# Kernel optimization log

Hardware: AMD Instinct MI355X
Metric: run time of the kernel (lower is better)

The kernel has to match this reference:

```python
import jax, jax.numpy as jnp
import numpy as np
from jax import lax

T, H, F, E, K = 4096, 1024, 2048, 8, 2

def setup_inputs() -> dict:
    key = jax.random.key(0)
    k1, k2, k3, k4 = jax.random.split(key, 4)
    return {
        "hidden_states": jax.random.normal(k1, (T, H), jnp.float32),
        "gate_w": jax.random.normal(k2, (E, H), jnp.float32) * 0.02,
        "w1": jax.random.normal(k3, (E, 2 * F, H), jnp.float32) * 0.02,  # fused gate+up
        "w2": jax.random.normal(k4, (E, H, F), jnp.float32) * 0.02,      # down proj
        "top_k": K,
    }

def reference(hidden_states, gate_w, w1, w2, top_k):
    tokens = hidden_states.shape[0]
    # Router gate (Linear, no bias)
    router_logits = hidden_states @ gate_w.T                     # [T, E]
    probs = jax.nn.softmax(router_logits.astype(jnp.float32), axis=-1)
    topk_w, topk_idx = lax.top_k(probs, top_k)                   # [T, K]
    topk_w = topk_w / jnp.sum(topk_w, axis=-1, keepdims=True)    # renormalize
    # Dense combine weights [T, E] (zero for unselected experts)
    combine = jnp.zeros_like(probs).at[jnp.arange(tokens)[:, None], topk_idx].add(topk_w)
    combine = combine.astype(hidden_states.dtype)

    def expert_step(acc, ew):
        w1_e, w2_e, c_e = ew                                     # [2F,H], [H,F], [T]
        h = hidden_states @ w1_e.T                               # [T, 2F]
        g, u = jnp.split(h, 2, axis=-1)
        y = (jax.nn.silu(g) * u) @ w2_e.T                        # [T, H]
        return acc + c_e[:, None] * y, None

    acc0 = jnp.zeros_like(hidden_states)
    final_hidden_states, _ = lax.scan(expert_step, acc0, (w1, w2, combine.T))
    return final_hidden_states, router_logits
```

## Files before the change

kernel.cpp:

```cpp
#include <hip/hip_runtime.h>

#define T 4096
#define Hdim 1024
#define Fdim 2048
#define NE 8
#define TOPK 2
#define TK (T*TOPK)

typedef unsigned short ushort_t;
typedef __attribute__((ext_vector_type(8))) short bf16x8;
typedef __attribute__((ext_vector_type(4))) float floatx4;

__device__ __forceinline__ ushort_t f2bf(float f) {
    unsigned u = __float_as_uint(f);
    u += 0x7fff + ((u >> 16) & 1);
    return (ushort_t)(u >> 16);
}
__device__ __forceinline__ uint4 cvt8(const float4 a, const float4 b) {
    uint4 r;
    r.x = (unsigned)f2bf(a.x) | ((unsigned)f2bf(a.y) << 16);
    r.y = (unsigned)f2bf(a.z) | ((unsigned)f2bf(a.w) << 16);
    r.z = (unsigned)f2bf(b.x) | ((unsigned)f2bf(b.y) << 16);
    r.w = (unsigned)f2bf(b.z) | ((unsigned)f2bf(b.w) << 16);
    return r;
}
__device__ __forceinline__ void gld16(const ushort_t* g, short* l) {
    __builtin_amdgcn_global_load_lds((const __attribute__((address_space(1))) void*)g,
                                     (__attribute__((address_space(3))) void*)l, 16, 0, 0);
}

__global__ __launch_bounds__(256) void cvt2_kernel(
    const float* __restrict__ srcA, ushort_t* __restrict__ dstA, long n8A,
    const float* __restrict__ srcB, ushort_t* __restrict__ dstB)
{
    long i = (long)blockIdx.x * 256 + threadIdx.x;
    if (i < n8A) {
        float4 a = *(const float4*)(srcA + i * 8);
        float4 b = *(const float4*)(srcA + i * 8 + 4);
        *(uint4*)(dstA + i * 8) = cvt8(a, b);
    } else {
        long j = i - n8A;
        float4 a = *(const float4*)(srcB + j * 8);
        float4 b = *(const float4*)(srcB + j * 8 + 4);
        *(uint4*)(dstB + j * 8) = cvt8(a, b);
    }
}

__global__ __launch_bounds__(256) void cvt_kernel(const float* __restrict__ src,
                                                  ushort_t* __restrict__ dst)
{
    long i = (long)blockIdx.x * 256 + threadIdx.x;
    float4 a = *(const float4*)(src + i * 8);
    float4 b = *(const float4*)(src + i * 8 + 4);
    *(uint4*)(dst + i * 8) = cvt8(a, b);
}

__global__ __launch_bounds__(64) void router_kernel(
    const float* __restrict__ hs, const float* __restrict__ gw,
    float* __restrict__ logits_out,
    int2* __restrict__ choice, float2* __restrict__ cwt, int* __restrict__ counts)
{
    const int t = blockIdx.x;
    const int lane = threadIdx.x;
    if (t == 0 && lane < NE) counts[lane] = 0;

    float hreg[16];
#pragma unroll
    for (int i = 0; i < 16; ++i)
        hreg[i] = hs[(long)t * Hdim + lane + 64 * i];

    float acc[NE];
#pragma unroll
    for (int e = 0; e < NE; ++e) {
        float s = 0.f;
#pragma unroll
        for (int i = 0; i < 16; ++i)
            s += hreg[i] * gw[e * Hdim + lane + 64 * i];
#pragma unroll
        for (int off = 32; off > 0; off >>= 1)
            s += __shfl_xor(s, off, 64);
        acc[e] = s;
    }

    if (lane < NE) logits_out[t * NE + lane] = acc[lane];

    if (lane == 0) {
        int i1 = 0;
#pragma unroll
        for (int e = 1; e < NE; ++e) if (acc[e] > acc[i1]) i1 = e;
        int i2 = -1;
#pragma unroll
        for (int e = 0; e < NE; ++e) {
            if (e == i1) continue;
            if (i2 < 0 || acc[e] > acc[i2]) i2 = e;
        }
        float p2 = __expf(acc[i2] - acc[i1]);
        float z  = 1.f + p2;
        choice[t] = make_int2(i1, i2);
        cwt[t]    = make_float2(1.f / z, p2 / z);
    }
}

__global__ __launch_bounds__(256) void scatter_kernel(
    const int2* __restrict__ choice, const float2* __restrict__ cwt,
    int* __restrict__ counts, int* __restrict__ tok_slot, float* __restrict__ tok_wt)
{
    __shared__ int lhist[NE];
    __shared__ int lbase[NE];
    __shared__ int lpos[NE];
    const int tid = threadIdx.x;
    if (tid < NE) { lhist[tid] = 0; lpos[tid] = 0; }
    __syncthreads();

    const int t = blockIdx.x * 256 + tid;
    int2   ch = choice[t];
    float2 wv = cwt[t];
    atomicAdd(&lhist[ch.x], 1);
    atomicAdd(&lhist[ch.y], 1);
    __syncthreads();

    if (tid < NE) lbase[tid] = atomicAdd(&counts[tid], lhist[tid]);
    __syncthreads();

    int p1 = atomicAdd(&lpos[ch.x], 1);
    int p2 = atomicAdd(&lpos[ch.y], 1);
    int o1 = lbase[ch.x] + p1;
    int o2 = lbase[ch.y] + p2;
    tok_slot[ch.x * T + o1] = t * TOPK + 0;
    tok_wt [ch.x * T + o1] = wv.x;
    tok_slot[ch.y * T + o2] = t * TOPK + 1;
    tok_wt [ch.y * T + o2] = wv.y;
}

__global__ __launch_bounds__(256) void gemm1_kernel(
    const ushort_t* __restrict__ hsb, const ushort_t* __restrict__ w1b,
    const int* __restrict__ counts, const int* __restrict__ tok_slot,
    ushort_t* __restrict__ actb)
{
    const int e = blockIdx.z;
    const int cnt = counts[e];
    const int row0 = blockIdx.y * 128;
    if (row0 >= cnt) return;
    const int f0 = blockIdx.x * 64;

    __shared__ short As[128 * 32];
    __shared__ short Bs[128 * 32];
    __shared__ int slotLds[128];

    const int tid = threadIdx.x;
    if (tid < 128) {
        int idx = row0 + tid;
        slotLds[tid] = (idx < cnt) ? tok_slot[e * T + idx] : -1;
    }
    __syncthreads();

    const int rA0 = tid >> 2,      rA1 = 64 + (tid >> 2);
    const int seg = (tid & 3) * 8;
    int s0 = slotLds[rA0], s1 = slotLds[rA1];
    const ushort_t* srcA0 = hsb + (long)((s0 >= 0 ? (s0 >> 1) : 0)) * Hdim + seg;
    const ushort_t* srcA1 = hsb + (long)((s1 >= 0 ? (s1 >> 1) : 0)) * Hdim + seg;
    const ushort_t* srcB0 = w1b + ((long)e * 2 * Fdim + (f0 + rA0)) * Hdim + seg;
    const ushort_t* srcB1 = w1b + ((long)e * 2 * Fdim + Fdim + (f0 + rA0)) * Hdim + seg;

    const int lane = tid & 63;
    const int w = tid >> 6;
    const int wm = (w >> 1) * 64;
    const int wn = (w & 1) * 32;
    const int fr = lane & 15, fg = lane >> 4;

    floatx4 accg[4][2] = {};
    floatx4 accu[4][2] = {};

    for (int k0 = 0; k0 < Hdim; k0 += 32) {
        __syncthreads();
        gld16(srcA0 + k0, &As[tid * 8]);
        gld16(srcA1 + k0, &As[(256 + tid) * 8]);
        gld16(srcB0 + k0, &Bs[tid * 8]);
        gld16(srcB1 + k0, &Bs[(256 + tid) * 8]);
        __syncthreads();

        bf16x8 a[4], g[2], u[2];
#pragma unroll
        for (int ms = 0; ms < 4; ++ms)
            a[ms] = *(bf16x8*)&As[(wm + ms * 16 + fr) * 32 + fg * 8];
#pragma unroll
        for (int ns = 0; ns < 2; ++ns) {
            g[ns] = *(bf16x8*)&Bs[(wn + ns * 16 + fr) * 32 + fg * 8];
            u[ns] = *(bf16x8*)&Bs[(64 + wn + ns * 16 + fr) * 32 + fg * 8];
        }
#pragma unroll
        for (int ms = 0; ms < 4; ++ms)
#pragma unroll
            for (int ns = 0; ns < 2; ++ns) {
                accg[ms][ns] = __builtin_amdgcn_mfma_f32_16x16x32_bf16(a[ms], g[ns], accg[ms][ns], 0, 0, 0);
                accu[ms][ns] = __builtin_amdgcn_mfma_f32_16x16x32_bf16(a[ms], u[ns], accu[ms][ns], 0, 0, 0);
            }
    }

#pragma unroll
    for (int ms = 0; ms < 4; ++ms)
#pragma unroll
        for (int ns = 0; ns < 2; ++ns)
#pragma unroll
            for (int j = 0; j < 4; ++j) {
                int m = wm + ms * 16 + fg * 4 + j;
                int slot = slotLds[m];
                if (slot >= 0) {
                    int fcol = f0 + wn + ns * 16 + fr;
                    float gv = accg[ms][ns][j];
                    float uv = accu[ms][ns][j];
                    float av = (gv / (1.f + __expf(-gv))) * uv;
                    actb[(long)slot * Fdim + fcol] = f2bf(av);
                }
            }
}

__global__ __launch_bounds__(512) void gemm2_kernel(
    const ushort_t* __restrict__ actb, const ushort_t* __restrict__ w2b,
    const int* __restrict__ counts, const int* __restrict__ tok_slot,
    const float* __restrict__ tok_wt, float* __restrict__ partial)
{
    const int e = blockIdx.z;
    const int cnt = counts[e];
    const int row0 = blockIdx.y * 128;
    if (row0 >= cnt) return;
    const int h0 = blockIdx.x * 128;

    __shared__ short As[128 * 32];
    __shared__ short Bs[128 * 32];
    __shared__ int   slotLds[128];
    __shared__ float wtLds[128];

    const int tid = threadIdx.x;
    if (tid < 128) {
        int idx = row0 + tid;
        bool ok = idx < cnt;
        slotLds[tid] = ok ? tok_slot[e * T + idx] : -1;
        wtLds[tid]   = ok ? tok_wt [e * T + idx] : 0.f;
    }
    __syncthreads();

    const int r   = tid >> 2;
    const int seg = (tid & 3) * 8;
    int s = slotLds[r];
    const ushort_t* srcA = actb + (long)(s >= 0 ? s : 0) * Fdim + seg;
    const ushort_t* srcB = w2b + ((long)e * Hdim + (h0 + r)) * Fdim + seg;

    const int lane = tid & 63;
    const int w = tid >> 6;
    const int wm = (w >> 2) * 64;
    const int wn = (w & 3) * 32;
    const int fr = lane & 15, fg = lane >> 4;

    floatx4 acc[4][2] = {};

    for (int k0 = 0; k0 < Fdim; k0 += 32) {
        __syncthreads();
        gld16(srcA + k0, &As[tid * 8]);
        gld16(srcB + k0, &Bs[tid * 8]);
        __syncthreads();

        bf16x8 a[4], b[2];
#pragma unroll
        for (int ms = 0; ms < 4; ++ms)
            a[ms] = *(bf16x8*)&As[(wm + ms * 16 + fr) * 32 + fg * 8];
#pragma unroll
        for (int ns = 0; ns < 2; ++ns)
            b[ns] = *(bf16x8*)&Bs[(wn + ns * 16 + fr) * 32 + fg * 8];
#pragma unroll
        for (int ms = 0; ms < 4; ++ms)
#pragma unroll
            for (int ns = 0; ns < 2; ++ns)
                acc[ms][ns] = __builtin_amdgcn_mfma_f32_16x16x32_bf16(a[ms], b[ns], acc[ms][ns], 0, 0, 0);
    }

#pragma unroll
    for (int ms = 0; ms < 4; ++ms)
#pragma unroll
        for (int ns = 0; ns < 2; ++ns)
#pragma unroll
            for (int j = 0; j < 4; ++j) {
                int m = wm + ms * 16 + fg * 4 + j;
                int slot = slotLds[m];
                if (slot >= 0) {
                    int hcol = h0 + wn + ns * 16 + fr;
                    partial[(long)slot * Hdim + hcol] = acc[ms][ns][j] * wtLds[m];
                }
            }
}

__global__ __launch_bounds__(256) void combine_kernel(
    const float* __restrict__ partial, float* __restrict__ out)
{
    long i = (long)blockIdx.x * 256 + threadIdx.x;
    int t  = (int)(i / (Hdim / 4));
    int h4 = (int)(i % (Hdim / 4));
    const float4 p0 = *(const float4*)&partial[(long)(2 * t    ) * Hdim + h4 * 4];
    const float4 p1 = *(const float4*)&partial[(long)(2 * t + 1) * Hdim + h4 * 4];
    float4 s;
    s.x = p0.x + p1.x; s.y = p0.y + p1.y; s.z = p0.z + p1.z; s.w = p0.w + p1.w;
    *(float4*)&out[(long)t * Hdim + h4 * 4] = s;
}

extern "C" void kernel_launch(void* const* d_in, const int* in_sizes, int n_in,
                              void* d_out, int out_size, void* d_ws, size_t ws_size,
                              hipStream_t stream)
{
    const float* hs = (const float*)d_in[0];
    const float* gw = (const float*)d_in[1];
    const float* w1 = (const float*)d_in[2];
    const float* w2 = (const float*)d_in[3];

    float* out        = (float*)d_out;
    float* logits_out = out + (long)T * Hdim;

    char* ws = (char*)d_ws;
    size_t off = 0;
    int* counts = (int*)(ws + off);          off += 256;
    int* tok_slot = (int*)(ws + off);        off += (size_t)NE * T * sizeof(int);
    float* tok_wt = (float*)(ws + off);      off += (size_t)NE * T * sizeof(float);
    off = (off + 255) & ~(size_t)255;
    ushort_t* hsb = (ushort_t*)(ws + off);   off += (size_t)T * Hdim * sizeof(ushort_t);
    off = (off + 255) & ~(size_t)255;
    char* w1region = ws + off;               off += (size_t)NE * 2 * Fdim * Hdim * sizeof(ushort_t);
    ushort_t* w1b = (ushort_t*)w1region;
    ushort_t* w2b = (ushort_t*)w1region;
    float* partial = (float*)(w1region + (size_t)NE * Hdim * Fdim * sizeof(ushort_t));
    off = (off + 255) & ~(size_t)255;
    ushort_t* actb = (ushort_t*)(ws + off);  off += (size_t)TK * Fdim * sizeof(ushort_t);
    int2*   choice = (int2*)actb;
    float2* cwt    = (float2*)((char*)actb + (size_t)T * sizeof(int2));

    const long n8_hs = (long)T * Hdim / 8;
    const long n8_w1 = (long)NE * 2 * Fdim * Hdim / 8;
    const long n8_w2 = (long)NE * Hdim * Fdim / 8;

    cvt2_kernel<<<(int)((n8_hs + n8_w1) / 256), 256, 0, stream>>>(hs, hsb, n8_hs, w1, w1b);
    router_kernel<<<T, 64, 0, stream>>>(hs, gw, logits_out, choice, cwt, counts);
    scatter_kernel<<<T / 256, 256, 0, stream>>>(choice, cwt, counts, tok_slot, tok_wt);
    gemm1_kernel<<<dim3(Fdim / 64, T / 128, NE), 256, 0, stream>>>(hsb, w1b, counts, tok_slot, actb);
    cvt_kernel<<<(int)(n8_w2 / 256), 256, 0, stream>>>(w2, w2b);
    gemm2_kernel<<<dim3(Hdim / 128, T / 128, NE), 512, 0, stream>>>(actb, w2b, counts, tok_slot, tok_wt, partial);
    combine_kernel<<<(int)((long)T * Hdim / 4 / 256), 256, 0, stream>>>(partial, out);
}
```

Before: 437.3 us.

## Split-K the down-projection GEMM with atomic accumulation and retile its warps

The down-projection GEMM now splits the F reduction into two halves, each handled by its own block, and accumulates results into the partial buffer with float atomics. The partial buffer is zeroed in the same kernel that converts w2 to bf16. Blocks drop from 512 to 256 threads, with each warp computing a 64x64 sub-tile instead of 64x32, so each thread loads two rows of the A and B tiles. The gate/up GEMM is also issued as two launches over halves of F. The aim is more parallel blocks and more MFMA reuse per LDS load, at the cost of atomic traffic, an extra 32MB zeroing pass and more accumulator registers.

```diff
diff --git a/kernel.cpp b/kernel.cpp
--- a/kernel.cpp
+++ b/kernel.cpp
@@ -46,13 +46,21 @@
     }
 }
 
-__global__ __launch_bounds__(256) void cvt_kernel(const float* __restrict__ src,
-                                                  ushort_t* __restrict__ dst)
+__global__ __launch_bounds__(256) void cvtw2_zero_kernel(
+    const float* __restrict__ src, ushort_t* __restrict__ dst, long n8,
+    float* __restrict__ partial)
 {
     long i = (long)blockIdx.x * 256 + threadIdx.x;
-    float4 a = *(const float4*)(src + i * 8);
-    float4 b = *(const float4*)(src + i * 8 + 4);
-    *(uint4*)(dst + i * 8) = cvt8(a, b);
+    if (i < n8) {
+        float4 a = *(const float4*)(src + i * 8);
+        float4 b = *(const float4*)(src + i * 8 + 4);
+        *(uint4*)(dst + i * 8) = cvt8(a, b);
+    } else {
+        long j = i - n8;
+        float4 z = make_float4(0.f, 0.f, 0.f, 0.f);
+        *(float4*)(partial + j * 8)     = z;
+        *(float4*)(partial + j * 8 + 4) = z;
+    }
 }
 
 __global__ __launch_bounds__(64) void router_kernel(
@@ -135,13 +143,13 @@
 __global__ __launch_bounds__(256) void gemm1_kernel(
     const ushort_t* __restrict__ hsb, const ushort_t* __restrict__ w1b,
     const int* __restrict__ counts, const int* __restrict__ tok_slot,
-    ushort_t* __restrict__ actb)
+    ushort_t* __restrict__ actb, int f_base)
 {
     const int e = blockIdx.z;
     const int cnt = counts[e];
     const int row0 = blockIdx.y * 128;
     if (row0 >= cnt) return;
-    const int f0 = blockIdx.x * 64;
+    const int f0 = f_base + blockIdx.x * 64;
 
     __shared__ short As[128 * 32];
     __shared__ short Bs[128 * 32];
@@ -215,7 +223,7 @@
             }
 }
 
-__global__ __launch_bounds__(512) void gemm2_kernel(
+__global__ __launch_bounds__(256) void gemm2_kernel(
     const ushort_t* __restrict__ actb, const ushort_t* __restrict__ w2b,
     const int* __restrict__ counts, const int* __restrict__ tok_slot,
     const float* __restrict__ tok_wt, float* __restrict__ partial)
@@ -224,7 +232,9 @@
     const int cnt = counts[e];
     const int row0 = blockIdx.y * 128;
     if (row0 >= cnt) return;
-    const int h0 = blockIdx.x * 128;
+    const int ks = blockIdx.x & 1;
+    const int h0 = (blockIdx.x >> 1) * 128;
+    const int kbase = ks * (Fdim / 2);
 
     __shared__ short As[128 * 32];
     __shared__ short Bs[128 * 32];
@@ -240,51 +250,55 @@
     }
     __syncthreads();
 
-    const int r   = tid >> 2;
+    const int rA0 = tid >> 2, rA1 = 64 + (tid >> 2);
     const int seg = (tid & 3) * 8;
-    int s = slotLds[r];
-    const ushort_t* srcA = actb + (long)(s >= 0 ? s : 0) * Fdim + seg;
-    const ushort_t* srcB = w2b + ((long)e * Hdim + (h0 + r)) * Fdim + seg;
+    int s0 = slotLds[rA0], s1 = slotLds[rA1];
+    const ushort_t* srcA0 = actb + (long)(s0 >= 0 ? s0 : 0) * Fdim + kbase + seg;
+    const ushort_t* srcA1 = actb + (long)(s1 >= 0 ? s1 : 0) * Fdim + kbase + seg;
+    const ushort_t* srcB0 = w2b + ((long)e * Hdim + (h0 + rA0)) * Fdim + kbase + seg;
+    const ushort_t* srcB1 = w2b + ((long)e * Hdim + (h0 + rA1)) * Fdim + kbase + seg;
 
     const int lane = tid & 63;
     const int w = tid >> 6;
-    const int wm = (w >> 2) * 64;
-    const int wn = (w & 3) * 32;
+    const int wm = (w >> 1) * 64;
+    const int wn = (w & 1) * 64;
     const int fr = lane & 15, fg = lane >> 4;
 
-    floatx4 acc[4][2] = {};
-
-    for (int k0 = 0; k0 < Fdim; k0 += 32) {
+    floatx4 acc[4][4] = {};
+
+    for (int k0 = 0; k0 < Fdim / 2; k0 += 32) {
         __syncthreads();
-        gld16(srcA + k0, &As[tid * 8]);
-        gld16(srcB + k0, &Bs[tid * 8]);
+        gld16(srcA0 + k0, &As[tid * 8]);
+        gld16(srcA1 + k0, &As[(256 + tid) * 8]);
+        gld16(srcB0 + k0, &Bs[tid * 8]);
+        gld16(srcB1 + k0, &Bs[(256 + tid) * 8]);
         __syncthreads();
 
-        bf16x8 a[4], b[2];
+        bf16x8 a[4], b[4];
 #pragma unroll
         for (int ms = 0; ms < 4; ++ms)
             a[ms] = *(bf16x8*)&As[(wm + ms * 16 + fr) * 32 + fg * 8];
 #pragma unroll
-        for (int ns = 0; ns < 2; ++ns)
+        for (int ns = 0; ns < 4; ++ns)
             b[ns] = *(bf16x8*)&Bs[(wn + ns * 16 + fr) * 32 + fg * 8];
 #pragma unroll
         for (int ms = 0; ms < 4; ++ms)
 #pragma unroll
-            for (int ns = 0; ns < 2; ++ns)
+            for (int ns = 0; ns < 4; ++ns)
                 acc[ms][ns] = __builtin_amdgcn_mfma_f32_16x16x32_bf16(a[ms], b[ns], acc[ms][ns], 0, 0, 0);
     }
 
 #pragma unroll
     for (int ms = 0; ms < 4; ++ms)
 #pragma unroll
-        for (int ns = 0; ns < 2; ++ns)
+        for (int ns = 0; ns < 4; ++ns)
 #pragma unroll
             for (int j = 0; j < 4; ++j) {
                 int m = wm + ms * 16 + fg * 4 + j;
                 int slot = slotLds[m];
                 if (slot >= 0) {
                     int hcol = h0 + wn + ns * 16 + fr;
-                    partial[(long)slot * Hdim + hcol] = acc[ms][ns][j] * wtLds[m];
+                    atomicAdd(&partial[(long)slot * Hdim + hcol], acc[ms][ns][j] * wtLds[m]);
                 }
             }
 }
@@ -334,12 +348,14 @@
     const long n8_hs = (long)T * Hdim / 8;
     const long n8_w1 = (long)NE * 2 * Fdim * Hdim / 8;
     const long n8_w2 = (long)NE * Hdim * Fdim / 8;
+    const long n8_pz = (long)TK * Hdim / 8;
 
     cvt2_kernel<<<(int)((n8_hs + n8_w1) / 256), 256, 0, stream>>>(hs, hsb, n8_hs, w1, w1b);
     router_kernel<<<T, 64, 0, stream>>>(hs, gw, logits_out, choice, cwt, counts);
     scatter_kernel<<<T / 256, 256, 0, stream>>>(choice, cwt, counts, tok_slot, tok_wt);
-    gemm1_kernel<<<dim3(Fdim / 64, T / 128, NE), 256, 0, stream>>>(hsb, w1b, counts, tok_slot, actb);
-    cvt_kernel<<<(int)(n8_w2 / 256), 256, 0, stream>>>(w2, w2b);
-    gemm2_kernel<<<dim3(Hdim / 128, T / 128, NE), 512, 0, stream>>>(actb, w2b, counts, tok_slot, tok_wt, partial);
+    gemm1_kernel<<<dim3(Fdim / 128, T / 128, NE), 256, 0, stream>>>(hsb, w1b, counts, tok_slot, actb, 0);
+    gemm1_kernel<<<dim3(Fdim / 128, T / 128, NE), 256, 0, stream>>>(hsb, w1b, counts, tok_slot, actb, Fdim / 2);
+    cvtw2_zero_kernel<<<(int)((n8_w2 + n8_pz) / 256), 256, 0, stream>>>(w2, w2b, n8_w2, partial);
+    gemm2_kernel<<<dim3((Hdim / 128) * 2, T / 128, NE), 256, 0, stream>>>(actb, w2b, counts, tok_slot, tok_wt, partial);
     combine_kernel<<<(int)((long)T * Hdim / 4 / 256), 256, 0, stream>>>(partial, out);
 }
```

Result: slower. 489.4 us (+11.9%).

## Double GEMM K-tile to 64 with XOR-swizzled LDS; fuse hs bf16 cast into router

Applied to the files above, without the earlier changes.

Both expert GEMMs now stage 64-wide K tiles instead of 32, which halves the number of barrier-separated load/compute iterations. Columns in LDS are XOR-swizzled by row to avoid bank conflicts on the wider rows. The hidden-state bf16 conversion moves into the router kernel, which already reads hs, so the combined conversion kernel now only converts w1. The cost is doubled LDS per block, which may reduce occupancy, plus more address registers.

```diff
diff --git a/kernel.cpp b/kernel.cpp
--- a/kernel.cpp
+++ b/kernel.cpp
@@ -29,23 +29,6 @@
                                      (__attribute__((address_space(3))) void*)l, 16, 0, 0);
 }
 
-__global__ __launch_bounds__(256) void cvt2_kernel(
-    const float* __restrict__ srcA, ushort_t* __restrict__ dstA, long n8A,
-    const float* __restrict__ srcB, ushort_t* __restrict__ dstB)
-{
-    long i = (long)blockIdx.x * 256 + threadIdx.x;
-    if (i < n8A) {
-        float4 a = *(const float4*)(srcA + i * 8);
-        float4 b = *(const float4*)(srcA + i * 8 + 4);
-        *(uint4*)(dstA + i * 8) = cvt8(a, b);
-    } else {
-        long j = i - n8A;
-        float4 a = *(const float4*)(srcB + j * 8);
-        float4 b = *(const float4*)(srcB + j * 8 + 4);
-        *(uint4*)(dstB + j * 8) = cvt8(a, b);
-    }
-}
-
 __global__ __launch_bounds__(256) void cvt_kernel(const float* __restrict__ src,
                                                   ushort_t* __restrict__ dst)
 {
@@ -57,7 +40,7 @@
 
 __global__ __launch_bounds__(64) void router_kernel(
     const float* __restrict__ hs, const float* __restrict__ gw,
-    float* __restrict__ logits_out,
+    float* __restrict__ logits_out, ushort_t* __restrict__ hsb,
     int2* __restrict__ choice, float2* __restrict__ cwt, int* __restrict__ counts)
 {
     const int t = blockIdx.x;
@@ -68,6 +51,10 @@
 #pragma unroll
     for (int i = 0; i < 16; ++i)
         hreg[i] = hs[(long)t * Hdim + lane + 64 * i];
+
+#pragma unroll
+    for (int i = 0; i < 16; ++i)
+        hsb[(long)t * Hdim + lane + 64 * i] = f2bf(hreg[i]);
 
     float acc[NE];
 #pragma unroll
@@ -143,8 +130,8 @@
     if (row0 >= cnt) return;
     const int f0 = blockIdx.x * 64;
 
-    __shared__ short As[128 * 32];
-    __shared__ short Bs[128 * 32];
+    __shared__ short As[128 * 64];
+    __shared__ short Bs[128 * 64];
     __shared__ int slotLds[128];
 
     const int tid = threadIdx.x;
@@ -154,47 +141,58 @@
     }
     __syncthreads();
 
-    const int rA0 = tid >> 2,      rA1 = 64 + (tid >> 2);
-    const int seg = (tid & 3) * 8;
-    int s0 = slotLds[rA0], s1 = slotLds[rA1];
-    const ushort_t* srcA0 = hsb + (long)((s0 >= 0 ? (s0 >> 1) : 0)) * Hdim + seg;
-    const ushort_t* srcA1 = hsb + (long)((s1 >= 0 ? (s1 >> 1) : 0)) * Hdim + seg;
-    const ushort_t* srcB0 = w1b + ((long)e * 2 * Fdim + (f0 + rA0)) * Hdim + seg;
-    const ushort_t* srcB1 = w1b + ((long)e * 2 * Fdim + Fdim + (f0 + rA0)) * Hdim + seg;
+    const ushort_t* srcA[4];
+    const ushort_t* srcB[4];
+#pragma unroll
+    for (int i = 0; i < 4; ++i) {
+        int ci = i * 256 + tid;
+        int r  = ci >> 3;
+        int gc = (ci & 7) ^ (r & 7);
+        int s  = slotLds[r];
+        srcA[i] = hsb + (long)(s >= 0 ? (s >> 1) : 0) * Hdim + gc * 8;
+        long frow = (r < 64) ? (long)(f0 + r) : (long)(Fdim + f0 + (r - 64));
+        srcB[i] = w1b + ((long)e * 2 * Fdim + frow) * Hdim + gc * 8;
+    }
 
     const int lane = tid & 63;
     const int w = tid >> 6;
     const int wm = (w >> 1) * 64;
     const int wn = (w & 1) * 32;
     const int fr = lane & 15, fg = lane >> 4;
+    const int cs0 = (fg ^ (fr & 7)) * 8;
+    const int cs1 = ((4 + fg) ^ (fr & 7)) * 8;
 
     floatx4 accg[4][2] = {};
     floatx4 accu[4][2] = {};
 
-    for (int k0 = 0; k0 < Hdim; k0 += 32) {
+    for (int k0 = 0; k0 < Hdim; k0 += 64) {
         __syncthreads();
-        gld16(srcA0 + k0, &As[tid * 8]);
-        gld16(srcA1 + k0, &As[(256 + tid) * 8]);
-        gld16(srcB0 + k0, &Bs[tid * 8]);
-        gld16(srcB1 + k0, &Bs[(256 + tid) * 8]);
+#pragma unroll
+        for (int i = 0; i < 4; ++i) gld16(srcA[i] + k0, &As[(i * 256 + tid) * 8]);
+#pragma unroll
+        for (int i = 0; i < 4; ++i) gld16(srcB[i] + k0, &Bs[(i * 256 + tid) * 8]);
         __syncthreads();
 
-        bf16x8 a[4], g[2], u[2];
-#pragma unroll
-        for (int ms = 0; ms < 4; ++ms)
-            a[ms] = *(bf16x8*)&As[(wm + ms * 16 + fr) * 32 + fg * 8];
-#pragma unroll
-        for (int ns = 0; ns < 2; ++ns) {
-            g[ns] = *(bf16x8*)&Bs[(wn + ns * 16 + fr) * 32 + fg * 8];
-            u[ns] = *(bf16x8*)&Bs[(64 + wn + ns * 16 + fr) * 32 + fg * 8];
+#pragma unroll
+        for (int kk = 0; kk < 2; ++kk) {
+            const int cs = kk ? cs1 : cs0;
+            bf16x8 a[4], g[2], u[2];
+#pragma unroll
+            for (int ms = 0; ms < 4; ++ms)
+                a[ms] = *(bf16x8*)&As[(wm + ms * 16 + fr) * 64 + cs];
+#pragma unroll
+            for (int ns = 0; ns < 2; ++ns) {
+                g[ns] = *(bf16x8*)&Bs[(wn + ns * 16 + fr) * 64 + cs];
+                u[ns] = *(bf16x8*)&Bs[(64 + wn + ns * 16 + fr) * 64 + cs];
+            }
+#pragma unroll
+            for (int ms = 0; ms < 4; ++ms)
+#pragma unroll
+                for (int ns = 0; ns < 2; ++ns) {
+                    accg[ms][ns] = __builtin_amdgcn_mfma_f32_16x16x32_bf16(a[ms], g[ns], accg[ms][ns], 0, 0, 0);
+                    accu[ms][ns] = __builtin_amdgcn_mfma_f32_16x16x32_bf16(a[ms], u[ns], accu[ms][ns], 0, 0, 0);
+                }
         }
-#pragma unroll
-        for (int ms = 0; ms < 4; ++ms)
-#pragma unroll
-            for (int ns = 0; ns < 2; ++ns) {
-                accg[ms][ns] = __builtin_amdgcn_mfma_f32_16x16x32_bf16(a[ms], g[ns], accg[ms][ns], 0, 0, 0);
-                accu[ms][ns] = __builtin_amdgcn_mfma_f32_16x16x32_bf16(a[ms], u[ns], accu[ms][ns], 0, 0, 0);
-            }
     }
 
 #pragma unroll
@@ -226,8 +224,8 @@
     if (row0 >= cnt) return;
     const int h0 = blockIdx.x * 128;
 
-    __shared__ short As[128 * 32];
-    __shared__ short Bs[128 * 32];
+    __shared__ short As[128 * 64];
+    __shared__ short Bs[128 * 64];
     __shared__ int   slotLds[128];
     __shared__ float wtLds[128];
 
@@ -240,38 +238,52 @@
     }
     __syncthreads();
 
-    const int r   = tid >> 2;
-    const int seg = (tid & 3) * 8;
-    int s = slotLds[r];
-    const ushort_t* srcA = actb + (long)(s >= 0 ? s : 0) * Fdim + seg;
-    const ushort_t* srcB = w2b + ((long)e * Hdim + (h0 + r)) * Fdim + seg;
+    const ushort_t* srcA[2];
+    const ushort_t* srcB[2];
+#pragma unroll
+    for (int i = 0; i < 2; ++i) {
+        int ci = i * 512 + tid;
+        int r  = ci >> 3;
+        int gc = (ci & 7) ^ (r & 7);
+        int s  = slotLds[r];
+        srcA[i] = actb + (long)(s >= 0 ? s : 0) * Fdim + gc * 8;
+        srcB[i] = w2b + ((long)e * Hdim + (h0 + r)) * Fdim + gc * 8;
+    }
 
     const int lane = tid & 63;
     const int w = tid >> 6;
     const int wm = (w >> 2) * 64;
     const int wn = (w & 3) * 32;
     const int fr = lane & 15, fg = lane >> 4;
+    const int cs0 = (fg ^ (fr & 7)) * 8;
+    const int cs1 = ((4 + fg) ^ (fr & 7)) * 8;
 
     floatx4 acc[4][2] = {};
 
-    for (int k0 = 0; k0 < Fdim; k0 += 32) {
+    for (int k0 = 0; k0 < Fdim; k0 += 64) {
         __syncthreads();
-        gld16(srcA + k0, &As[tid * 8]);
-        gld16(srcB + k0, &Bs[tid * 8]);
+        gld16(srcA[0] + k0, &As[tid * 8]);
+        gld16(srcA[1] + k0, &As[(512 + tid) * 8]);
+        gld16(srcB[0] + k0, &Bs[tid * 8]);
+        gld16(srcB[1] + k0, &Bs[(512 + tid) * 8]);
         __syncthreads();
 
-        bf16x8 a[4], b[2];
-#pragma unroll
-        for (int ms = 0; ms < 4; ++ms)
-            a[ms] = *(bf16x8*)&As[(wm + ms * 16 + fr) * 32 + fg * 8];
-#pragma unroll
-        for (int ns = 0; ns < 2; ++ns)
-            b[ns] = *(bf16x8*)&Bs[(wn + ns * 16 + fr) * 32 + fg * 8];
-#pragma unroll
-        for (int ms = 0; ms < 4; ++ms)
+#pragma unroll
+        for (int kk = 0; kk < 2; ++kk) {
+            const int cs = kk ? cs1 : cs0;
+            bf16x8 a[4], b[2];
+#pragma unroll
+            for (int ms = 0; ms < 4; ++ms)
+                a[ms] = *(bf16x8*)&As[(wm + ms * 16 + fr) * 64 + cs];
 #pragma unroll
             for (int ns = 0; ns < 2; ++ns)
-                acc[ms][ns] = __builtin_amdgcn_mfma_f32_16x16x32_bf16(a[ms], b[ns], acc[ms][ns], 0, 0, 0);
+                b[ns] = *(bf16x8*)&Bs[(wn + ns * 16 + fr) * 64 + cs];
+#pragma unroll
+            for (int ms = 0; ms < 4; ++ms)
+#pragma unroll
+                for (int ns = 0; ns < 2; ++ns)
+                    acc[ms][ns] = __builtin_amdgcn_mfma_f32_16x16x32_bf16(a[ms], b[ns], acc[ms][ns], 0, 0, 0);
+        }
     }
 
 #pragma unroll
@@ -331,12 +343,11 @@
     int2*   choice = (int2*)actb;
     float2* cwt    = (float2*)((char*)actb + (size_t)T * sizeof(int2));
 
-    const long n8_hs = (long)T * Hdim / 8;
     const long n8_w1 = (long)NE * 2 * Fdim * Hdim / 8;
     const long n8_w2 = (long)NE * Hdim * Fdim / 8;
 
-    cvt2_kernel<<<(int)((n8_hs + n8_w1) / 256), 256, 0, stream>>>(hs, hsb, n8_hs, w1, w1b);
-    router_kernel<<<T, 64, 0, stream>>>(hs, gw, logits_out, choice, cwt, counts);
+    cvt_kernel<<<(int)(n8_w1 / 256), 256, 0, stream>>>(w1, w1b);
+    router_kernel<<<T, 64, 0, stream>>>(hs, gw, logits_out, hsb, choice, cwt, counts);
     scatter_kernel<<<T / 256, 256, 0, stream>>>(choice, cwt, counts, tok_slot, tok_wt);
     gemm1_kernel<<<dim3(Fdim / 64, T / 128, NE), 256, 0, stream>>>(hsb, w1b, counts, tok_slot, actb);
     cvt_kernel<<<(int)(n8_w2 / 256), 256, 0, stream>>>(w2, w2b);
```

Result: no change. 433.6 us (-0.8%).
